# Optimization experiments

Hardware: AMD Instinct MI355X
Metric: run time of the kernel (lower is better)

The kernel has to match this reference:

```python
import jax, jax.numpy as jnp
import numpy as np

WIN_H, WIN_W = 7, 7
NUM_HEADS = 16
DIM = 512
HEAD_DIM = DIM // NUM_HEADS
SCALE = HEAD_DIM ** -0.5


def rel_pos_index(h, w):
    # Faithful port of get_relative_position_index
    xx, yy = jnp.meshgrid(jnp.arange(h), jnp.arange(w), indexing='ij')
    coords = jnp.stack([yy, xx], axis=0).reshape(2, -1)  # (2, N)
    rel = coords[:, :, None] - coords[:, None, :]        # (2, N, N)
    return (rel[0] + h - 1) * (2 * w - 1) + (rel[1] + w - 1)  # (N, N)


def setup_inputs() -> dict:
    key = jax.random.key(0)
    ks = jax.random.split(key, 5)
    B_, N, C = 4096, WIN_H * WIN_W, DIM
    num_win = 64
    return {
        'x': jax.random.normal(ks[0], (B_, N, C), dtype=jnp.float32),
        'mask': jnp.zeros((num_win, N, N), dtype=jnp.float32),  # 0/-inf shift mask; zeros = no shift
        'qkv_w': jax.random.normal(ks[1], (C, 3 * C), dtype=jnp.float32) * 0.02,
        'qkv_b': jnp.zeros((3 * C,), dtype=jnp.float32),
        'proj_w': jax.random.normal(ks[2], (C, C), dtype=jnp.float32) * 0.02,
        'proj_b': jnp.zeros((C,), dtype=jnp.float32),
        'bias_table': jax.random.normal(ks[3], ((2 * WIN_H - 1) * (2 * WIN_W - 1), NUM_HEADS), dtype=jnp.float32) * 0.02,
    }


def reference(x, mask, qkv_w, qkv_b, proj_w, proj_b, bias_table):
    B_, N, C = x.shape
    H, hd = NUM_HEADS, HEAD_DIM
    qkv = x @ qkv_w + qkv_b                                  # (B_, N, 3C)
    qkv = qkv.reshape(B_, N, 3, H, hd).transpose(2, 0, 3, 1, 4)  # (3, B_, H, N, hd)
    q, k, v = qkv[0], qkv[1], qkv[2]
    q = q * jnp.asarray(SCALE, dtype=qkv.dtype)
    attn = jnp.einsum('bhnd,bhmd->bhnm', q, k)               # (B_, H, N, N)
    idx = rel_pos_index(WIN_H, WIN_W)                        # (N, N)
    bias = bias_table[idx].transpose(2, 0, 1)                # (H, N, N)
    attn = attn + bias
    num_win = mask.shape[0]
    attn = attn.reshape(B_ // num_win, num_win, H, N, N) + mask[None, :, None]
    attn = jax.nn.softmax(attn.reshape(B_, H, N, N), axis=-1)
    out = jnp.einsum('bhnm,bhmd->bhnd', attn, v)             # (B_, H, N, hd)
    out = out.transpose(0, 2, 1, 3).reshape(B_, N, C)
    return out @ proj_w + proj_b
```

## Files before the change

kernel.cpp:

```cpp
#include <hip/hip_runtime.h>
#include <stdint.h>

#define WIN_N 49
#define NH 16
#define HD 32
#define CDIM 512
#define NB 4096
#define M_ROWS (NB * WIN_N)
#define QKV_N 1536
#define SCALE_Q 0.17677669529663689f

typedef __attribute__((ext_vector_type(8))) short bf16x8;
typedef __attribute__((ext_vector_type(4))) float f32x4;

__device__ __forceinline__ unsigned short f2bf(float f) {
  unsigned int u = __float_as_uint(f);
  u += 0x7fff + ((u >> 16) & 1);
  return (unsigned short)(u >> 16);
}
__device__ __forceinline__ unsigned int pack2(float a, float b) {
  return (unsigned int)f2bf(a) | ((unsigned int)f2bf(b) << 16);
}

typedef const __attribute__((address_space(1))) unsigned int* gas1_t;
typedef __attribute__((address_space(3))) unsigned int* las3_t;
#define GL2LDS(g, l) __builtin_amdgcn_global_load_lds((gas1_t)(g), (las3_t)(l), 16, 0, 0)

__global__ __launch_bounds__(256) void prep_w_t(const float* __restrict__ src,
                                                unsigned short* __restrict__ dst,
                                                int RS, int CS) {
  __shared__ float T[64][65];
  const int tid = threadIdx.x;
  const int k0 = blockIdx.y * 64;
  const int n0 = blockIdx.x * 64;
  const int c = tid & 63;
#pragma unroll
  for (int rr = 0; rr < 16; rr++) {
    const int row = rr * 4 + (tid >> 6);
    T[row][c] = src[(size_t)(k0 + row) * CS + n0 + c];
  }
  __syncthreads();
#pragma unroll
  for (int wr = 0; wr < 16; wr++) {
    const int n = wr * 4 + (tid >> 6);
    dst[(size_t)(n0 + n) * RS + k0 + c] = f2bf(T[c][n]);
  }
}

template <bool A_F32, bool OUT_F32>
__global__ __launch_bounds__(256) void gemm_bt(
    const void* __restrict__ Aptr, int lda,
    const unsigned short* __restrict__ Bt,
    void* __restrict__ Cptr, int ldc,
    const float* __restrict__ bias,
    int K, int scale_cols, float scale) {
  __shared__ __align__(16) unsigned short SB[4][4096];
  const int tid = threadIdx.x;

  const int gx = gridDim.x;
  const int nwg = gx * gridDim.y;
  int lin = blockIdx.y * gx + blockIdx.x;
  lin = (lin & 7) * (nwg >> 3) + (lin >> 3);
  const int bm = (lin / gx) * 128;
  const int bn = (lin % gx) * 128;

  const int lane = tid & 63, wid = tid >> 6;
  const int wm = (wid & 1) * 64, wn = (wid >> 1) * 64;
  const int quad = lane >> 4, l16 = lane & 15;
  const int sRd = quad ^ ((l16 >> 1) & 3);

  const f32x4 fzero = {0.f, 0.f, 0.f, 0.f};
  f32x4 acc[4][4];
#pragma unroll
  for (int i = 0; i < 4; i++)
#pragma unroll
    for (int j = 0; j < 4; j++) acc[i][j] = fzero;

  const int rS = tid >> 2;
  const int sS = (tid & 3) ^ ((tid >> 3) & 3);
  const float* pAf = (const float*)Aptr + (size_t)(bm + rS) * lda + sS * 8;
  const unsigned short* pAb = (const unsigned short*)Aptr + (size_t)(bm + rS) * lda + sS * 8;
  const unsigned short* pB0 = Bt + (size_t)(bn + rS) * K + sS * 8;
  const size_t a64 = (size_t)64 * lda;
  const size_t b64 = (size_t)64 * K;
  const int dsA0 = rS * 32 + (tid & 3) * 8;
  const int dsA1 = (rS + 64) * 32 + (tid & 3) * 8;

#define COMPUTE(ab, bb)                                                          \
  do {                                                                           \
    bf16x8 a[4], b[4];                                                           \
    _Pragma("unroll") for (int i = 0; i < 4; i++)                                \
        a[i] = *(const bf16x8*)&SB[ab][(wm + i * 16 + l16) * 32 + sRd * 8];      \
    _Pragma("unroll") for (int i = 0; i < 4; i++)                                \
        b[i] = *(const bf16x8*)&SB[bb][(wn + i * 16 + l16) * 32 + sRd * 8];      \
    _Pragma("unroll") for (int i = 0; i < 4; i++)                                \
        _Pragma("unroll") for (int j = 0; j < 4; j++)                            \
            acc[i][j] = __builtin_amdgcn_mfma_f32_16x16x32_bf16(a[i], b[j],      \
                                                                acc[i][j], 0, 0, 0); \
  } while (0)

  if constexpr (A_F32) {
    for (int kk = 0; kk < K; kk += 32) {
      const float* p0 = pAf + kk;
      float4 x0 = *(const float4*)p0;
      float4 x1 = *(const float4*)(p0 + 4);
      float4 y0 = *(const float4*)(p0 + a64);
      float4 y1 = *(const float4*)(p0 + a64 + 4);
      *(uint4*)&SB[0][dsA0] =
          make_uint4(pack2(x0.x, x0.y), pack2(x0.z, x0.w), pack2(x1.x, x1.y), pack2(x1.z, x1.w));
      *(uint4*)&SB[0][dsA1] =
          make_uint4(pack2(y0.x, y0.y), pack2(y0.z, y0.w), pack2(y1.x, y1.y), pack2(y1.z, y1.w));
      GL2LDS(pB0 + kk, &SB[1][wid * 512]);
      GL2LDS(pB0 + kk + b64, &SB[1][2048 + wid * 512]);
      __syncthreads();
      COMPUTE(0, 1);
      __syncthreads();
    }
  } else {
#define STAGE(ab, bb, kk_)                                   \
  do {                                                       \
    GL2LDS(pAb + (kk_), &SB[ab][wid * 512]);                 \
    GL2LDS(pAb + (kk_) + a64, &SB[ab][2048 + wid * 512]);    \
    GL2LDS(pB0 + (kk_), &SB[bb][wid * 512]);                 \
    GL2LDS(pB0 + (kk_) + b64, &SB[bb][2048 + wid * 512]);    \
  } while (0)
    const int nt = K >> 5;
    STAGE(0, 1, 0);
    for (int t = 0; t < nt; t += 2) {
      __syncthreads();
      STAGE(2, 3, (t + 1) * 32);
      COMPUTE(0, 1);
      __syncthreads();
      if (t + 2 < nt) STAGE(0, 1, (t + 2) * 32);
      COMPUTE(2, 3);
    }
#undef STAGE
  }
#undef COMPUTE

  if constexpr (OUT_F32) {
#pragma unroll
    for (int i = 0; i < 4; i++) {
      const int row = bm + wm + i * 16 + quad * 4;
#pragma unroll
      for (int j = 0; j < 4; j++) {
        const int col = bn + wn + j * 16 + l16;
        const float bv = bias[col];
#pragma unroll
        for (int r = 0; r < 4; r++)
          ((float*)Cptr)[(size_t)(row + r) * ldc + col] = acc[i][j][r] + bv;
      }
    }
  } else {
    unsigned short* Ct = &SB[0][0];
    __syncthreads();
#pragma unroll
    for (int i = 0; i < 4; i++) {
#pragma unroll
      for (int j = 0; j < 4; j++) {
        const int colg = bn + wn + j * 16 + l16;
        const float bv = bias[colg];
        const float sc = (colg < scale_cols) ? scale : 1.0f;
        const int coll = wn + j * 16 + l16;
#pragma unroll
        for (int r = 0; r < 4; r++) {
          const int rowl = wm + i * 16 + quad * 4 + r;
          Ct[rowl * 128 + coll] = f2bf((acc[i][j][r] + bv) * sc);
        }
      }
    }
    __syncthreads();
#pragma unroll
    for (int tt = 0; tt < 8; tt++) {
      const int row = tt * 16 + (tid >> 4);
      const int ce = (tid & 15) * 8;
      uint4 vv = *(const uint4*)&Ct[row * 128 + ce];
      *(uint4*)&((unsigned short*)Cptr)[(size_t)(bm + row) * ldc + bn + ce] = vv;
    }
  }
}

__global__ __launch_bounds__(256) void attn_mfma(
    unsigned short* __restrict__ qkv,
    const float* __restrict__ bias_table,
    const float* __restrict__ mask) {
  const int PS = 72;
  const int VS = 64;
  __shared__ __align__(16) unsigned short Pl_all[4][64 * 72];
  __shared__ __align__(16) unsigned short Vt_all[4][32 * 64];
  const int tid = threadIdx.x;
  const int wid = tid >> 6, lane = tid & 63;
  const int quad = lane >> 4, l16 = lane & 15;
  const int b = blockIdx.x;
  const int h = blockIdx.y * 4 + wid;
  unsigned short* Pl = Pl_all[wid];
  unsigned short* Vt = Vt_all[wid];
  const size_t row0 = (size_t)b * WIN_N;

  bf16x8 aq[4], bk[4];
#pragma unroll
  for (int i = 0; i < 4; i++) {
    size_t r = row0 + i * 16 + l16;
    if (r > (size_t)(M_ROWS - 1)) r = M_ROWS - 1;
    const unsigned short* pq = qkv + r * QKV_N + h * HD + quad * 8;
    aq[i] = *(const bf16x8*)pq;
    bk[i] = *(const bf16x8*)(pq + 512);
  }

  {
    const int m = lane;
    if (m < WIN_N) {
      const unsigned short* pv = qkv + (row0 + m) * QKV_N + 1024 + h * HD;
      uint4 tv[4];
      tv[0] = *(const uint4*)(pv + 0);
      tv[1] = *(const uint4*)(pv + 8);
      tv[2] = *(const uint4*)(pv + 16);
      tv[3] = *(const uint4*)(pv + 24);
      const unsigned short* tmp = (const unsigned short*)tv;
#pragma unroll
      for (int d = 0; d < 32; d++) Vt[d * VS + m] = tmp[d];
    } else {
#pragma unroll
      for (int d = 0; d < 32; d++) Vt[d * VS + m] = 0;
    }
  }

  const f32x4 fzero = {0.f, 0.f, 0.f, 0.f};
  f32x4 s[4][4];
#pragma unroll
  for (int i = 0; i < 4; i++)
#pragma unroll
    for (int j = 0; j < 4; j++)
      s[i][j] = __builtin_amdgcn_mfma_f32_16x16x32_bf16(aq[i], bk[j], fzero, 0, 0, 0);

  const float* mrow = mask + (size_t)(b & 63) * (WIN_N * WIN_N);
#pragma unroll
  for (int i = 0; i < 4; i++) {
#pragma unroll
    for (int r = 0; r < 4; r++) {
      const int t = i * 16 + quad * 4 + r;
      const int ti = t / 7, tj = t % 7;
      float v[4];
#pragma unroll
      for (int j = 0; j < 4; j++) {
        const int m = j * 16 + l16;
        float x = s[i][j][r];
        if (t < WIN_N && m < WIN_N) {
          const int mi = m / 7, mj = m % 7;
          const int idx = (tj - mj + 6) * 13 + (ti - mi + 6);
          x += bias_table[idx * NH + h] + mrow[t * WIN_N + m];
        }
        if (m >= WIN_N) x = -3.0e38f;
        v[j] = x;
      }
      float mx = fmaxf(fmaxf(v[0], v[1]), fmaxf(v[2], v[3]));
      mx = fmaxf(mx, __shfl_xor(mx, 1));
      mx = fmaxf(mx, __shfl_xor(mx, 2));
      mx = fmaxf(mx, __shfl_xor(mx, 4));
      mx = fmaxf(mx, __shfl_xor(mx, 8));
      float p[4];
      float sum = 0.f;
#pragma unroll
      for (int j = 0; j < 4; j++) {
        p[j] = __expf(v[j] - mx);
        sum += p[j];
      }
      sum += __shfl_xor(sum, 1);
      sum += __shfl_xor(sum, 2);
      sum += __shfl_xor(sum, 4);
      sum += __shfl_xor(sum, 8);
      const float inv = 1.0f / sum;
#pragma unroll
      for (int j = 0; j < 4; j++) Pl[t * PS + j * 16 + l16] = f2bf(p[j] * inv);
    }
  }
  __syncthreads();

  f32x4 o[4][2];
#pragma unroll
  for (int i = 0; i < 4; i++)
#pragma unroll
    for (int ni = 0; ni < 2; ni++) o[i][ni] = fzero;
#pragma unroll
  for (int ki = 0; ki < 2; ki++) {
    bf16x8 bv[2];
#pragma unroll
    for (int ni = 0; ni < 2; ni++)
      bv[ni] = *(const bf16x8*)&Vt[(ni * 16 + l16) * VS + ki * 32 + quad * 8];
#pragma unroll
    for (int i = 0; i < 4; i++) {
      bf16x8 ap = *(const bf16x8*)&Pl[(i * 16 + l16) * PS + ki * 32 + quad * 8];
#pragma unroll
      for (int ni = 0; ni < 2; ni++)
        o[i][ni] = __builtin_amdgcn_mfma_f32_16x16x32_bf16(ap, bv[ni], o[i][ni], 0, 0, 0);
    }
  }

  unsigned short* Ol = Pl;
#pragma unroll
  for (int i = 0; i < 4; i++)
#pragma unroll
    for (int ni = 0; ni < 2; ni++)
#pragma unroll
      for (int r = 0; r < 4; r++)
        Ol[(i * 16 + quad * 4 + r) * 32 + ni * 16 + l16] = f2bf(o[i][ni][r]);
#pragma unroll
  for (int p = 0; p < 4; p++) {
    const int row = p * 16 + (lane >> 2);
    if (row < WIN_N) {
      const int ce = (lane & 3) * 8;
      uint4 vv = *(const uint4*)&Ol[row * 32 + ce];
      *(uint4*)(qkv + (row0 + row) * QKV_N + h * HD + ce) = vv;
    }
  }
}

extern "C" void kernel_launch(void* const* d_in, const int* in_sizes, int n_in,
                              void* d_out, int out_size, void* d_ws, size_t ws_size,
                              hipStream_t stream) {
  const float* x = (const float*)d_in[0];
  const float* mask = (const float*)d_in[1];
  const float* qkv_w = (const float*)d_in[2];
  const float* qkv_b = (const float*)d_in[3];
  const float* proj_w = (const float*)d_in[4];
  const float* proj_b = (const float*)d_in[5];
  const float* bias_table = (const float*)d_in[6];
  float* out = (float*)d_out;

  unsigned short* qkvb = (unsigned short*)d_ws;
  unsigned short* wqkv_t = qkvb + (size_t)M_ROWS * QKV_N;
  unsigned short* wproj_t = wqkv_t + (size_t)QKV_N * CDIM;

  prep_w_t<<<dim3(QKV_N / 64, CDIM / 64), 256, 0, stream>>>(qkv_w, wqkv_t, CDIM, QKV_N);
  prep_w_t<<<dim3(CDIM / 64, CDIM / 64), 256, 0, stream>>>(proj_w, wproj_t, CDIM, CDIM);

  gemm_bt<true, false><<<dim3(QKV_N / 128, M_ROWS / 128), 256, 0, stream>>>(
      x, CDIM, wqkv_t, qkvb, QKV_N, qkv_b, CDIM, 512, SCALE_Q);

  attn_mfma<<<dim3(NB, NH / 4), 256, 0, stream>>>(qkvb, bias_table, mask);

  gemm_bt<false, true><<<dim3(CDIM / 128, M_ROWS / 128), 256, 0, stream>>>(
      qkvb, QKV_N, wproj_t, out, CDIM, proj_b, CDIM, 0, 1.0f);
}
```

Measured before the change: 1.854 ms.

## Pre-convert x to bf16, precompute bias+mask table, drop softmax max

A separate kernel converts x to bf16 so the QKV GEMM can use the double-buffered direct global-to-LDS path instead of the unpipelined fp32 load-and-pack loop. A second kernel precomputes a combined relative-position-bias plus mask table per window and head, with padding columns set to -30. The attention softmax drops the row-max subtraction and reads the table directly. Both scratch buffers live in the output buffer before it is written. Skipping the max subtraction removes shuffles but risks overflow if logits are large, and the extra passes add memory traffic.

```diff
diff --git a/kernel.cpp b/kernel.cpp
--- a/kernel.cpp
+++ b/kernel.cpp
@@ -47,9 +47,39 @@
   }
 }
 
-template <bool A_F32, bool OUT_F32>
+__global__ __launch_bounds__(256) void prep_combo(
+    const float* __restrict__ bias_table, const float* __restrict__ mask,
+    float* __restrict__ combo) {
+  const int e = blockIdx.x * 256 + threadIdx.x;
+  const int m = e & 63, t = (e >> 6) & 63, h = (e >> 12) & 15, g = e >> 16;
+  float v = 0.f;
+  if (t < WIN_N) {
+    if (m < WIN_N) {
+      const int ti = t / 7, tj = t % 7, mi = m / 7, mj = m % 7;
+      const int idx = (tj - mj + 6) * 13 + (ti - mi + 6);
+      v = bias_table[idx * NH + h] + mask[(size_t)g * (WIN_N * WIN_N) + t * WIN_N + m];
+    } else {
+      v = -30.0f;
+    }
+  }
+  combo[e] = v;
+}
+
+__global__ void conv_x(const float* __restrict__ x,
+                       unsigned short* __restrict__ xb, int n8) {
+  int i = blockIdx.x * blockDim.x + threadIdx.x;
+  const int stride = gridDim.x * blockDim.x;
+  for (; i < n8; i += stride) {
+    const float4* p = (const float4*)(x + (size_t)i * 8);
+    float4 a = p[0], b = p[1];
+    *(uint4*)(xb + (size_t)i * 8) =
+        make_uint4(pack2(a.x, a.y), pack2(a.z, a.w), pack2(b.x, b.y), pack2(b.z, b.w));
+  }
+}
+
+template <bool OUT_F32>
 __global__ __launch_bounds__(256) void gemm_bt(
-    const void* __restrict__ Aptr, int lda,
+    const unsigned short* __restrict__ A, int lda,
     const unsigned short* __restrict__ Bt,
     void* __restrict__ Cptr, int ldc,
     const float* __restrict__ bias,
@@ -78,13 +108,18 @@
 
   const int rS = tid >> 2;
   const int sS = (tid & 3) ^ ((tid >> 3) & 3);
-  const float* pAf = (const float*)Aptr + (size_t)(bm + rS) * lda + sS * 8;
-  const unsigned short* pAb = (const unsigned short*)Aptr + (size_t)(bm + rS) * lda + sS * 8;
+  const unsigned short* pA0 = A + (size_t)(bm + rS) * lda + sS * 8;
   const unsigned short* pB0 = Bt + (size_t)(bn + rS) * K + sS * 8;
   const size_t a64 = (size_t)64 * lda;
   const size_t b64 = (size_t)64 * K;
-  const int dsA0 = rS * 32 + (tid & 3) * 8;
-  const int dsA1 = (rS + 64) * 32 + (tid & 3) * 8;
+
+#define STAGE(ab, bb, kk_)                                   \
+  do {                                                       \
+    GL2LDS(pA0 + (kk_), &SB[ab][wid * 512]);                 \
+    GL2LDS(pA0 + (kk_) + a64, &SB[ab][2048 + wid * 512]);    \
+    GL2LDS(pB0 + (kk_), &SB[bb][wid * 512]);                 \
+    GL2LDS(pB0 + (kk_) + b64, &SB[bb][2048 + wid * 512]);    \
+  } while (0)
 
 #define COMPUTE(ab, bb)                                                          \
   do {                                                                           \
@@ -99,43 +134,17 @@
                                                                 acc[i][j], 0, 0, 0); \
   } while (0)
 
-  if constexpr (A_F32) {
-    for (int kk = 0; kk < K; kk += 32) {
-      const float* p0 = pAf + kk;
-      float4 x0 = *(const float4*)p0;
-      float4 x1 = *(const float4*)(p0 + 4);
-      float4 y0 = *(const float4*)(p0 + a64);
-      float4 y1 = *(const float4*)(p0 + a64 + 4);
-      *(uint4*)&SB[0][dsA0] =
-          make_uint4(pack2(x0.x, x0.y), pack2(x0.z, x0.w), pack2(x1.x, x1.y), pack2(x1.z, x1.w));
-      *(uint4*)&SB[0][dsA1] =
-          make_uint4(pack2(y0.x, y0.y), pack2(y0.z, y0.w), pack2(y1.x, y1.y), pack2(y1.z, y1.w));
-      GL2LDS(pB0 + kk, &SB[1][wid * 512]);
-      GL2LDS(pB0 + kk + b64, &SB[1][2048 + wid * 512]);
-      __syncthreads();
-      COMPUTE(0, 1);
-      __syncthreads();
-    }
-  } else {
-#define STAGE(ab, bb, kk_)                                   \
-  do {                                                       \
-    GL2LDS(pAb + (kk_), &SB[ab][wid * 512]);                 \
-    GL2LDS(pAb + (kk_) + a64, &SB[ab][2048 + wid * 512]);    \
-    GL2LDS(pB0 + (kk_), &SB[bb][wid * 512]);                 \
-    GL2LDS(pB0 + (kk_) + b64, &SB[bb][2048 + wid * 512]);    \
-  } while (0)
-    const int nt = K >> 5;
-    STAGE(0, 1, 0);
-    for (int t = 0; t < nt; t += 2) {
-      __syncthreads();
-      STAGE(2, 3, (t + 1) * 32);
-      COMPUTE(0, 1);
-      __syncthreads();
-      if (t + 2 < nt) STAGE(0, 1, (t + 2) * 32);
-      COMPUTE(2, 3);
-    }
+  const int nt = K >> 5;
+  STAGE(0, 1, 0);
+  for (int t = 0; t < nt; t += 2) {
+    __syncthreads();
+    STAGE(2, 3, (t + 1) * 32);
+    COMPUTE(0, 1);
+    __syncthreads();
+    if (t + 2 < nt) STAGE(0, 1, (t + 2) * 32);
+    COMPUTE(2, 3);
+  }
 #undef STAGE
-  }
 #undef COMPUTE
 
   if constexpr (OUT_F32) {
@@ -182,8 +191,7 @@
 
 __global__ __launch_bounds__(256) void attn_mfma(
     unsigned short* __restrict__ qkv,
-    const float* __restrict__ bias_table,
-    const float* __restrict__ mask) {
+    const float* __restrict__ combo) {
   const int PS = 72;
   const int VS = 64;
   __shared__ __align__(16) unsigned short Pl_all[4][64 * 72];
@@ -233,36 +241,18 @@
     for (int j = 0; j < 4; j++)
       s[i][j] = __builtin_amdgcn_mfma_f32_16x16x32_bf16(aq[i], bk[j], fzero, 0, 0, 0);
 
-  const float* mrow = mask + (size_t)(b & 63) * (WIN_N * WIN_N);
+  const float* ch = combo + ((((b & 63) * NH + h) << 12) + l16);
 #pragma unroll
   for (int i = 0; i < 4; i++) {
 #pragma unroll
     for (int r = 0; r < 4; r++) {
       const int t = i * 16 + quad * 4 + r;
-      const int ti = t / 7, tj = t % 7;
-      float v[4];
-#pragma unroll
-      for (int j = 0; j < 4; j++) {
-        const int m = j * 16 + l16;
-        float x = s[i][j][r];
-        if (t < WIN_N && m < WIN_N) {
-          const int mi = m / 7, mj = m % 7;
-          const int idx = (tj - mj + 6) * 13 + (ti - mi + 6);
-          x += bias_table[idx * NH + h] + mrow[t * WIN_N + m];
-        }
-        if (m >= WIN_N) x = -3.0e38f;
-        v[j] = x;
-      }
-      float mx = fmaxf(fmaxf(v[0], v[1]), fmaxf(v[2], v[3]));
-      mx = fmaxf(mx, __shfl_xor(mx, 1));
-      mx = fmaxf(mx, __shfl_xor(mx, 2));
-      mx = fmaxf(mx, __shfl_xor(mx, 4));
-      mx = fmaxf(mx, __shfl_xor(mx, 8));
+      const float* cb = ch + (t << 6);
       float p[4];
       float sum = 0.f;
 #pragma unroll
       for (int j = 0; j < 4; j++) {
-        p[j] = __expf(v[j] - mx);
+        p[j] = __expf(s[i][j][r] + cb[j * 16]);
         sum += p[j];
       }
       sum += __shfl_xor(sum, 1);
@@ -331,14 +321,19 @@
   unsigned short* wqkv_t = qkvb + (size_t)M_ROWS * QKV_N;
   unsigned short* wproj_t = wqkv_t + (size_t)QKV_N * CDIM;
 
+  unsigned short* xb = (unsigned short*)d_out;
+  float* combo = (float*)((char*)d_out + (size_t)208 * 1024 * 1024);
+
   prep_w_t<<<dim3(QKV_N / 64, CDIM / 64), 256, 0, stream>>>(qkv_w, wqkv_t, CDIM, QKV_N);
   prep_w_t<<<dim3(CDIM / 64, CDIM / 64), 256, 0, stream>>>(proj_w, wproj_t, CDIM, CDIM);
-
-  gemm_bt<true, false><<<dim3(QKV_N / 128, M_ROWS / 128), 256, 0, stream>>>(
-      x, CDIM, wqkv_t, qkvb, QKV_N, qkv_b, CDIM, 512, SCALE_Q);
-
-  attn_mfma<<<dim3(NB, NH / 4), 256, 0, stream>>>(qkvb, bias_table, mask);
-
-  gemm_bt<false, true><<<dim3(CDIM / 128, M_ROWS / 128), 256, 0, stream>>>(
+  prep_combo<<<16384, 256, 0, stream>>>(bias_table, mask, combo);
+  conv_x<<<4096, 256, 0, stream>>>(x, xb, (M_ROWS * CDIM) / 8);
+
+  gemm_bt<false><<<dim3(QKV_N / 128, M_ROWS / 128), 256, 0, stream>>>(
+      xb, CDIM, wqkv_t, qkvb, QKV_N, qkv_b, CDIM, 512, SCALE_Q);
+
+  attn_mfma<<<dim3(NB, NH / 4), 256, 0, stream>>>(qkvb, combo);
+
+  gemm_bt<true><<<dim3(CDIM / 128, M_ROWS / 128), 256, 0, stream>>>(
       qkvb, QKV_N, wproj_t, out, CDIM, proj_b, CDIM, 0, 1.0f);
 }
```

Result: faster. 1.639 ms (-11.6%).
